# Performance work log

Hardware: AMD Instinct MI355X
Metric: run time of the kernel (lower is better)

The kernel has to match this reference:

```python
import jax, jax.numpy as jnp
import numpy as np

K = 40  # k_point

def lrelu(v):
    return jax.nn.leaky_relu(v, 0.2)

def graph_feature(x, k):
    # x: [B, C, N] -> edge features [B, 2C, N, k] = concat(x_j - x_i, x_i)
    xx = jnp.sum(x * x, axis=1)                          # [B,N]
    inner = jnp.einsum('bcn,bcm->bnm', x, x)             # [B,N,N]
    dist = 2.0 * inner - xx[:, :, None] - xx[:, None, :] # negative squared distance
    idx = jax.lax.top_k(dist, k)[1]                      # [B,N,k] nearest neighbors
    xt = jnp.transpose(x, (0, 2, 1))                     # [B,N,C]
    nbr = jax.vmap(lambda f, i: f[i])(xt, idx)           # [B,N,k,C] gather
    ctr = xt[:, :, None, :]
    feat = jnp.concatenate([nbr - ctr, jnp.broadcast_to(ctr, nbr.shape)], axis=-1)
    return jnp.transpose(feat, (0, 3, 1, 2))             # [B,2C,N,k]

def conv2(f, w):  # 1x1 conv2d, no bias
    return jnp.einsum('bcnk,oc->bonk', f, w)

def conv1(f, w):  # 1x1 conv1d, no bias
    return jnp.einsum('bcn,oc->bon', f, w)

def edge_block(x, ws, k):
    f = graph_feature(x, k)
    for w in ws:
        f = lrelu(conv2(f, w))
    return jnp.max(f, axis=-1)                           # max over k neighbors

def setup_inputs() -> dict:
    key = jax.random.key(0)
    ks = jax.random.split(key, 20)
    B, N, NCLS, NSEG, D = 8, 2048, 16, 50, 1024
    def w(kk, o, c, s=0.05):
        return jax.random.normal(kk, (o, c), jnp.float32) * s
    return {
        'x': jax.random.normal(ks[0], (B, 3, N), jnp.float32),
        'l': jax.random.uniform(ks[1], (B, NCLS), dtype=jnp.float32),
        't_c1': w(ks[2], 64, 6), 't_c2': w(ks[3], 128, 64), 't_c3': w(ks[4], 1024, 128),
        't_f1': w(ks[5], 512, 1024), 't_f2': w(ks[6], 256, 512),
        't_f3_w': w(ks[7], 9, 256, 0.01),
        't_f3_b': jnp.eye(3, dtype=jnp.float32).reshape(9),  # identity-transform init
        'b1a': w(ks[8], 64, 6), 'b1b': w(ks[9], 64, 64),
        'b2a': w(ks[10], 64, 128), 'b2b': w(ks[11], 64, 64),
        'b3a': w(ks[12], 64, 128),
        'm1': w(ks[13], D, 192), 'm2': w(ks[14], 64, NCLS),
        'h1': w(ks[15], 256, D + 256), 'h2': w(ks[16], 256, 256),
        'h3': w(ks[17], 128, 256), 'h4': w(ks[18], NSEG, 128),
    }

def reference(x, l, t_c1, t_c2, t_c3, t_f1, t_f2, t_f3_w, t_f3_b,
              b1a, b1b, b2a, b2b, b3a, m1, m2, h1, h2, h3, h4):
    B, _, N = x.shape
    # transform net on graph features of raw points
    x0 = graph_feature(x, K)                              # [B,6,N,K]
    t = lrelu(conv2(x0, t_c1))
    t = lrelu(conv2(t, t_c2))
    t = jnp.max(t, axis=-1)                               # [B,128,N]
    t = lrelu(conv1(t, t_c3))
    t = jnp.max(t, axis=-1)                               # [B,1024]
    t = lrelu(t @ t_f1.T)
    t = lrelu(t @ t_f2.T)
    T = (t @ t_f3_w.T + t_f3_b).reshape(B, 3, 3)
    x = jnp.einsum('bji,bjn->bin', T, x)                  # T^T @ x
    # edge-conv blocks
    x1 = edge_block(x, [b1a, b1b], K)                     # [B,64,N]
    x2 = edge_block(x1, [b2a, b2b], K)                    # [B,64,N]
    x3 = edge_block(x2, [b3a], K)                         # [B,64,N]
    cat = jnp.concatenate([x1, x2, x3], axis=1)           # [B,192,N]
    g = jnp.max(lrelu(conv1(cat, m1)), axis=-1, keepdims=True)  # [B,1024,1]
    lv = lrelu(jnp.einsum('bc,oc->bo', l, m2))[:, :, None]      # [B,64,1]
    glob = jnp.broadcast_to(jnp.concatenate([g, lv], axis=1), (B, g.shape[1] + 64, N))
    h = jnp.concatenate([glob, x1, x2, x3], axis=1)       # [B,1280,N]
    h = lrelu(conv1(h, h1))
    h = lrelu(conv1(h, h2))
    h = lrelu(conv1(h, h3))
    return conv1(h, h4)                                   # [B,50,N]
```

## Files before the change

kernel.cpp:

```cpp
#include <hip/hip_runtime.h>
#include <cstdint>

#define NPTS 2048
#define BATCH 8
#define KNN 40

__device__ __forceinline__ float lrelu(float v){ return fmaxf(v, 0.2f*v); }
__device__ __forceinline__ bool better(float v1,int i1,float v2,int i2){
  return (v1>v2) || (v1==v2 && i1<i2);
}
__device__ __forceinline__ float4 ld4(const float* p){ return *(const float4*)p; }

#define INSERT8(v,id,d,m) \
  if (better(d, m, v[7], id[7])){ \
    v[7]=d; id[7]=m; \
    { if (better(v[7],id[7],v[6],id[6])){ float tv=v[6];int ti=id[6]; v[6]=v[7];id[6]=id[7]; v[7]=tv;id[7]=ti; } } \
    { if (better(v[6],id[6],v[5],id[5])){ float tv=v[5];int ti=id[5]; v[5]=v[6];id[5]=id[6]; v[6]=tv;id[6]=ti; } } \
    { if (better(v[5],id[5],v[4],id[4])){ float tv=v[4];int ti=id[4]; v[4]=v[5];id[4]=id[5]; v[5]=tv;id[5]=ti; } } \
    { if (better(v[4],id[4],v[3],id[3])){ float tv=v[3];int ti=id[3]; v[3]=v[4];id[3]=id[4]; v[4]=tv;id[4]=ti; } } \
    { if (better(v[3],id[3],v[2],id[2])){ float tv=v[2];int ti=id[2]; v[2]=v[3];id[2]=id[3]; v[3]=tv;id[3]=ti; } } \
    { if (better(v[2],id[2],v[1],id[1])){ float tv=v[1];int ti=id[1]; v[1]=v[2];id[1]=id[2]; v[2]=tv;id[2]=ti; } } \
    { if (better(v[1],id[1],v[0],id[0])){ float tv=v[0];int ti=id[0]; v[0]=v[1];id[0]=id[1]; v[1]=tv;id[1]=ti; } } \
  }

__global__ void transpose_kernel(const float* __restrict__ src, float* __restrict__ dst,
                                 int R, int C, int ld, int off){
  int i = blockIdx.x*256 + threadIdx.x;
  if (i < R*C){ int r = i / C, c = i % C; dst[c*R + r] = src[r*ld + off + c]; }
}

template<int TAG>
__global__ void norms_rows_kernel(const float* __restrict__ x, float* __restrict__ xx, int N){
  int b = blockIdx.y; int n = blockIdx.x*256 + threadIdx.x;
  const float* xb = x + (size_t)b*3*N;
  float v0 = xb[n], v1 = xb[N+n], v2 = xb[2*N+n];
  xx[(size_t)b*N + n] = v0*v0 + v1*v1 + v2*v2;
}

template<int TAG>
__global__ void norms_cl_kernel(const float* __restrict__ f, int off, float* __restrict__ xx, int N){
  int b = blockIdx.y; int n = blockIdx.x*256 + threadIdx.x;
  const float4* p = (const float4*)(f + ((size_t)b*N + n)*192 + off);
  float s = 0.f;
#pragma unroll
  for (int q=0;q<16;q++){ float4 v = p[q]; s += v.x*v.x + v.y*v.y + v.z*v.z + v.w*v.w; }
  xx[(size_t)b*N + n] = s;
}

__device__ __forceinline__ void sort8(float (&v)[8], int (&id)[8]){
#define CE(a,bq) { if (better(v[bq],id[bq],v[a],id[a])){ float tv=v[a]; int ti=id[a]; v[a]=v[bq]; id[a]=id[bq]; v[bq]=tv; id[bq]=ti; } }
  CE(0,1) CE(2,3) CE(4,5) CE(6,7)
  CE(0,2) CE(1,3) CE(4,6) CE(5,7)
  CE(1,2) CE(5,6)
  CE(0,4) CE(1,5) CE(2,6) CE(3,7)
  CE(2,4) CE(3,5)
  CE(1,2) CE(3,4) CE(5,6)
#undef CE
}

template<int TAG>
__global__ __launch_bounds__(256) void knn3_kernel(
    const float* __restrict__ xrows, const float* __restrict__ xx,
    int* __restrict__ idxT, int N){
  const int b = blockIdx.y, tid = threadIdx.x;
  const int w = tid>>6, lane = tid&63;
  const int nq = blockIdx.x*4 + w;
  const float* xb = xrows + (size_t)b*3*N;
  const float* xxb = xx + (size_t)b*N;
  float c0 = xb[nq], c1 = xb[N+nq], c2 = xb[2*N+nq];
  float xxn = xxb[nq];
  float v[8]; int id[8];
#pragma unroll
  for (int j=0;j<8;j++){ v[j]=-__builtin_inff(); id[j]=0x7FFFFFFF; }
  for (int j=0;j<32;j++){
    int m = j*64 + lane;
    float s = c0*xb[m] + c1*xb[N+m] + c2*xb[2*N+m];
    float d = 2.f*s - xxn - xxb[m];
    INSERT8(v, id, d, m)
  }
  float lastv = 0.f; int lasti = 0;
  int win = 0;
  for (int r=0;r<KNN;r++){
    float bv = v[0]; int bi = id[0];
#pragma unroll
    for (int off=32; off; off>>=1){
      float ov = __shfl_xor(bv, off);
      int   oi = __shfl_xor(bi, off);
      if (better(ov, oi, bv, bi)){ bv = ov; bi = oi; }
    }
    if (lane == r) win = bi;
    if (id[0] == bi){
      lastv = v[0]; lasti = id[0];
#pragma unroll
      for (int j=0;j<7;j++){ v[j]=v[j+1]; id[j]=id[j+1]; }
      v[7] = -__builtin_inff(); id[7] = 0x7FFFFFFF;
      if (id[0] == 0x7FFFFFFF){
        float nv = -__builtin_inff(); int ni = 0x7FFFFFFF;
        for (int j=0;j<32;j++){
          int m = j*64 + lane;
          float s = c0*xb[m] + c1*xb[N+m] + c2*xb[2*N+m];
          float dd = 2.f*s - xxn - xxb[m];
          if (better(lastv, lasti, dd, m) && better(dd, m, nv, ni)){ nv=dd; ni=m; }
        }
        v[0] = nv; id[0] = ni;
      }
    }
  }
  if (lane < KNN) idxT[((size_t)b*KNN + lane)*N + nq] = win;
}

template<int TAG>
__global__ __launch_bounds__(256) void knn64_kernel(
    const float* __restrict__ featT, int featOff,
    const float* __restrict__ xx, int* __restrict__ idxT, int N){
  const int b = blockIdx.y, tid = threadIdx.x;
  const int w = tid>>6, lane = tid&63;
  __shared__ float cand[32*64];
  __shared__ float dist[4*2048];
  const float* fb = featT + featOff;
  const float* xxb = xx + (size_t)b*N;
  const int nq = blockIdx.x*4 + w;
  const int h = lane>>5;
  float4 ctr8[8];
  {
    const float4* cp = (const float4*)(fb + ((size_t)b*N + nq)*192);
#pragma unroll
    for (int q=0;q<8;q++) ctr8[q] = cp[h*8 + q];
  }
  float xxn = xxb[nq];
  float* dw = &dist[w*2048];
  float4 g[2];
#pragma unroll
  for (int r=0;r<2;r++){
    int k2 = tid + 256*r;
    int c = k2>>4, f = k2&15;
    g[r] = ld4(&fb[((size_t)b*N + c)*192 + 4*f]);
  }
  const int cc = lane&31, swz = cc&15, qb = h*8;
  for (int t=0;t<64;t++){
    __syncthreads();
#pragma unroll
    for (int r=0;r<2;r++){
      int k2 = tid + 256*r;
      int c = k2>>4, f = k2&15;
      *(float4*)&cand[(c<<6) + ((f ^ (c&15))<<2)] = g[r];
    }
    __syncthreads();
    if (t+1 < 64){
      int m0n = (t+1)*32;
#pragma unroll
      for (int r=0;r<2;r++){
        int k2 = tid + 256*r;
        int c = k2>>4, f = k2&15;
        g[r] = ld4(&fb[((size_t)b*N + m0n + c)*192 + 4*f]);
      }
    }
    float s0=0.f,s1=0.f,s2=0.f,s3=0.f;
#pragma unroll
    for (int j=0;j<8;j++){
      float4 mv = *(const float4*)&cand[(cc<<6) + (((qb + j) ^ swz)<<2)];
      s0 = fmaf(ctr8[j].x, mv.x, s0);
      s1 = fmaf(ctr8[j].y, mv.y, s1);
      s2 = fmaf(ctr8[j].z, mv.z, s2);
      s3 = fmaf(ctr8[j].w, mv.w, s3);
    }
    float p = (s0+s1)+(s2+s3);
    float tot = p + __shfl_xor(p, 32);
    if (h == (t&1)){
      int m = t*32 + cc;
      dw[(t>>1)*64 + lane] = 2.f*tot - xxn - xxb[m];
    }
  }
  float v[8]; int id[8];
#pragma unroll
  for (int j=0;j<8;j++){ v[j]=dw[j*64+lane]; id[j]=j*64+lane; }
  sort8(v, id);
#pragma unroll
  for (int gq=1; gq<4; gq++){
    float a[8]; int ai[8];
#pragma unroll
    for (int j=0;j<8;j++){ a[j]=dw[(gq*8+j)*64+lane]; ai[j]=(gq*8+j)*64+lane; }
    sort8(a, ai);
    float m_[8]; int mi_[8];
#pragma unroll
    for (int k=0;k<8;k++){
      if (better(a[7-k], ai[7-k], v[k], id[k])){ m_[k]=a[7-k]; mi_[k]=ai[7-k]; }
      else                                     { m_[k]=v[k];   mi_[k]=id[k]; }
    }
#define CEB(x,y) { if (better(m_[y],mi_[y],m_[x],mi_[x])){ float tv=m_[x];int ti=mi_[x]; m_[x]=m_[y];mi_[x]=mi_[y]; m_[y]=tv;mi_[y]=ti; } }
    CEB(0,4) CEB(1,5) CEB(2,6) CEB(3,7)
    CEB(0,2) CEB(1,3) CEB(4,6) CEB(5,7)
    CEB(0,1) CEB(2,3) CEB(4,5) CEB(6,7)
#undef CEB
#pragma unroll
    for (int k=0;k<8;k++){ v[k]=m_[k]; id[k]=mi_[k]; }
  }
  float lastv = 0.f; int lasti = 0;
  int win = 0;
  for (int r=0;r<KNN;r++){
    float bv = v[0]; int bi = id[0];
#pragma unroll
    for (int off=32; off; off>>=1){
      float ov = __shfl_xor(bv, off);
      int   oi = __shfl_xor(bi, off);
      if (better(ov, oi, bv, bi)){ bv = ov; bi = oi; }
    }
    if (lane == r) win = bi;
    if (id[0] == bi){
      lastv = v[0]; lasti = id[0];
#pragma unroll
      for (int j=0;j<7;j++){ v[j]=v[j+1]; id[j]=id[j+1]; }
      v[7] = -__builtin_inff(); id[7] = 0x7FFFFFFF;
      if (id[0] == 0x7FFFFFFF){
        float nv = -__builtin_inff(); int ni = 0x7FFFFFFF;
        for (int j=0;j<32;j++){
          float vv = dw[j*64 + lane]; int m = j*64 + lane;
          if (better(lastv, lasti, vv, m) && better(vv, m, nv, ni)){ nv=vv; ni=m; }
        }
        v[0] = nv; id[0] = ni;
      }
    }
  }
  if (lane < KNN) idxT[((size_t)b*KNN + lane)*N + nq] = win;
}


__global__ __launch_bounds__(256) void edgeA_kernel(
    const float* __restrict__ x, const int* __restrict__ idxT,
    const float* __restrict__ w1, const float* __restrict__ w2,
    float* __restrict__ tT, int N){
  __shared__ float w1aT[3*64];
  __shared__ float wd3T[3*64];
  __shared__ float w2T[64*128];
  __shared__ float aT3[4][3*16];
  __shared__ float s1T[4][64*16];
  const int tid = threadIdx.x, w = tid>>6, lane = tid&63;
  const int oq = lane&7, rg = lane>>3;
  const int o0 = oq*8, r0 = rg*2;
  const int b = blockIdx.y, n0 = blockIdx.x*16;
  for (int i=tid; i<192; i+=256){
    int o = i&63, c = i/64;
    float a = w1[o*6+c];
    w1aT[c*64+o] = a; wd3T[c*64+o] = w1[o*6+3+c] - a;
  }
  for (int i=tid; i<128*64; i+=256){
    int o = i>>6, c = i&63;
    w2T[c*128+o] = w2[o*64+c];
  }
  if (tid < 48){ int c = tid>>4, r = tid&15; aT3[0][c*16+r] = x[((size_t)b*3+c)*N + n0 + r]; }
  __syncthreads();
  float base[16];
#pragma unroll
  for (int i=0;i<16;i++) base[i]=0.f;
#pragma unroll
  for (int c=0;c<3;c++){
    float4 wA = ld4(&wd3T[c*64+o0]), wB = ld4(&wd3T[c*64+o0+4]);
    float2 av = *(const float2*)&aT3[0][c*16+r0];
    float wv[8] = {wA.x,wA.y,wA.z,wA.w,wB.x,wB.y,wB.z,wB.w};
    float rv[2] = {av.x,av.y};
#pragma unroll
    for (int oo=0;oo<8;oo++)
#pragma unroll
      for (int rr=0;rr<2;rr++) base[oo*2+rr] = fmaf(wv[oo], rv[rr], base[oo*2+rr]);
  }
  __syncthreads();
  float mx[32];
#pragma unroll
  for (int i=0;i<32;i++) mx[i] = -__builtin_inff();
  for (int it=0; it<10; it++){
    int k = it*4 + w;
    int m = idxT[((size_t)b*KNN + k)*N + n0 + (lane&15)];
    if (lane < 48){ int c = lane>>4; aT3[w][c*16 + (lane&15)] = x[((size_t)b*3+c)*N + m]; }
    float acc[16];
#pragma unroll
    for (int i=0;i<16;i++) acc[i] = base[i];
#pragma unroll
    for (int c=0;c<3;c++){
      float4 wA = ld4(&w1aT[c*64+o0]), wB = ld4(&w1aT[c*64+o0+4]);
      float2 av = *(const float2*)&aT3[w][c*16+r0];
      float wv[8] = {wA.x,wA.y,wA.z,wA.w,wB.x,wB.y,wB.z,wB.w};
      float rv[2] = {av.x,av.y};
#pragma unroll
      for (int oo=0;oo<8;oo++)
#pragma unroll
        for (int rr=0;rr<2;rr++) acc[oo*2+rr] = fmaf(wv[oo], rv[rr], acc[oo*2+rr]);
    }
#pragma unroll
    for (int oo=0;oo<8;oo++){
      float2 sv; sv.x = lrelu(acc[oo*2]); sv.y = lrelu(acc[oo*2+1]);
      *(float2*)&s1T[w][(o0+oo)*16 + r0] = sv;
    }
    float acc2[32];
#pragma unroll
    for (int i=0;i<32;i++) acc2[i]=0.f;
    for (int c=0;c<64;c++){
      float2 av = *(const float2*)&s1T[w][c*16 + r0];
#pragma unroll
      for (int p=0;p<4;p++){
        float4 wv = ld4(&w2T[c*128 + p*32 + oq*4]);
        acc2[p*8+0] = fmaf(wv.x, av.x, acc2[p*8+0]);
        acc2[p*8+1] = fmaf(wv.x, av.y, acc2[p*8+1]);
        acc2[p*8+2] = fmaf(wv.y, av.x, acc2[p*8+2]);
        acc2[p*8+3] = fmaf(wv.y, av.y, acc2[p*8+3]);
        acc2[p*8+4] = fmaf(wv.z, av.x, acc2[p*8+4]);
        acc2[p*8+5] = fmaf(wv.z, av.y, acc2[p*8+5]);
        acc2[p*8+6] = fmaf(wv.w, av.x, acc2[p*8+6]);
        acc2[p*8+7] = fmaf(wv.w, av.y, acc2[p*8+7]);
      }
    }
#pragma unroll
    for (int i=0;i<32;i++) mx[i] = fmaxf(mx[i], lrelu(acc2[i]));
  }
  __syncthreads();
#pragma unroll
  for (int rr=0;rr<2;rr++){
#pragma unroll
    for (int p=0;p<4;p++){
      float4 a = make_float4(mx[p*8+0+rr], mx[p*8+2+rr], mx[p*8+4+rr], mx[p*8+6+rr]);
      *(float4*)&w2T[w*2048 + (r0+rr)*128 + p*32 + oq*4] = a;
    }
  }
  __syncthreads();
  for (int i=tid; i<2048; i+=256){
    float vv = fmaxf(fmaxf(w2T[i], w2T[2048+i]), fmaxf(w2T[4096+i], w2T[6144+i]));
    int r = i>>7, o = i&127;
    tT[((size_t)b*N + n0 + r)*128 + o] = vv;
  }
}

__global__ __launch_bounds__(128) void edgeB_kernel(
    const float* __restrict__ xp, const int* __restrict__ idxT,
    const float* __restrict__ w1, const float* __restrict__ w2,
    float* __restrict__ catT, int N){
  __shared__ float w1aT[3*64];
  __shared__ float wd3T[3*64];
  __shared__ float w2T[64*64];
  __shared__ float aT3[2][3*32];
  __shared__ float s1T[2][64*32];
  const int tid = threadIdx.x, w = tid>>6, lane = tid&63;
  const int oq = lane&7, rg = lane>>3;
  const int o0 = oq*8, r0 = rg*4;
  const int b = blockIdx.y, n0 = blockIdx.x*32;
  for (int i=tid; i<192; i+=128){
    int o = i&63, c = i>>6;
    float a = w1[o*6+c], bb = w1[o*6+3+c];
    w1aT[c*64+o] = a; wd3T[c*64+o] = bb - a;
  }
  for (int i=tid; i<64*64; i+=128){
    int o = i>>6, c = i&63;
    w2T[c*64+o] = w2[o*64+c];
  }
  if (tid < 32){
#pragma unroll
    for (int c=0;c<3;c++) aT3[0][c*32+tid] = xp[((size_t)b*3+c)*N + n0 + tid];
  }
  __syncthreads();
  float base[32];
#pragma unroll
  for (int i=0;i<32;i++) base[i]=0.f;
#pragma unroll
  for (int c=0;c<3;c++){
    float4 w0 = ld4(&wd3T[c*64+o0]), w1v = ld4(&wd3T[c*64+o0+4]);
    float4 av = ld4(&aT3[0][c*32+r0]);
    float wv[8] = {w0.x,w0.y,w0.z,w0.w,w1v.x,w1v.y,w1v.z,w1v.w};
    float rv[4] = {av.x,av.y,av.z,av.w};
#pragma unroll
    for (int oo=0;oo<8;oo++)
#pragma unroll
      for (int rr=0;rr<4;rr++) base[oo*4+rr] = fmaf(wv[oo], rv[rr], base[oo*4+rr]);
  }
  __syncthreads();
  float mx[32];
#pragma unroll
  for (int i=0;i<32;i++) mx[i] = -__builtin_inff();
  for (int it=0; it<20; it++){
    int k = it*2 + w;
    {
      int row = lane&31;
      int m = idxT[((size_t)b*KNN + k)*N + n0 + row];
      if (lane < 32){
#pragma unroll
        for (int c=0;c<3;c++) aT3[w][c*32+row] = xp[((size_t)b*3+c)*N + m];
      }
    }
    float acc[32];
#pragma unroll
    for (int i=0;i<32;i++) acc[i] = base[i];
#pragma unroll
    for (int c=0;c<3;c++){
      float4 w0 = ld4(&w1aT[c*64+o0]), w1v = ld4(&w1aT[c*64+o0+4]);
      float4 av = ld4(&aT3[w][c*32+r0]);
      float wv[8] = {w0.x,w0.y,w0.z,w0.w,w1v.x,w1v.y,w1v.z,w1v.w};
      float rv[4] = {av.x,av.y,av.z,av.w};
#pragma unroll
      for (int oo=0;oo<8;oo++)
#pragma unroll
        for (int rr=0;rr<4;rr++) acc[oo*4+rr] = fmaf(wv[oo], rv[rr], acc[oo*4+rr]);
    }
#pragma unroll
    for (int oo=0;oo<8;oo++){
      float4 sv = make_float4(lrelu(acc[oo*4+0]), lrelu(acc[oo*4+1]), lrelu(acc[oo*4+2]), lrelu(acc[oo*4+3]));
      *(float4*)&s1T[w][(o0+oo)*32 + r0] = sv;
    }
    float acc2[32];
#pragma unroll
    for (int i=0;i<32;i++) acc2[i]=0.f;
    for (int c=0;c<64;c++){
      float4 w0 = ld4(&w2T[c*64+o0]), w1v = ld4(&w2T[c*64+o0+4]);
      float4 av = ld4(&s1T[w][c*32+r0]);
      float wv[8] = {w0.x,w0.y,w0.z,w0.w,w1v.x,w1v.y,w1v.z,w1v.w};
      float rv[4] = {av.x,av.y,av.z,av.w};
#pragma unroll
      for (int oo=0;oo<8;oo++)
#pragma unroll
        for (int rr=0;rr<4;rr++) acc2[oo*4+rr] = fmaf(wv[oo], rv[rr], acc2[oo*4+rr]);
    }
#pragma unroll
    for (int i=0;i<32;i++) mx[i] = fmaxf(mx[i], lrelu(acc2[i]));
  }
  __syncthreads();
#pragma unroll
  for (int rr=0;rr<4;rr++){
    float4 a = make_float4(mx[0*4+rr], mx[1*4+rr], mx[2*4+rr], mx[3*4+rr]);
    float4 bq = make_float4(mx[4*4+rr], mx[5*4+rr], mx[6*4+rr], mx[7*4+rr]);
    *(float4*)&s1T[w][(r0+rr)*64 + o0] = a;
    *(float4*)&s1T[w][(r0+rr)*64 + o0 + 4] = bq;
  }
  __syncthreads();
  for (int i=tid; i<2048; i+=128){
    float v = fmaxf(s1T[0][i], s1T[1][i]);
    int r = i>>6, o = i&63;
    catT[((size_t)b*N + n0 + r)*192 + o] = v;
  }
}

__global__ __launch_bounds__(128) void edgeC_kernel(
    const float* __restrict__ inT, int inOff, const int* __restrict__ idxT,
    const float* __restrict__ w1, const float* __restrict__ w2,
    float* __restrict__ catT, int outOff, int N){
  __shared__ float w1T[64*64];
  __shared__ float w2T[64*64];
  __shared__ float aT[2][64*32];
  __shared__ float s1T[2][64*32];
  const int tid = threadIdx.x, w = tid>>6, lane = tid&63;
  const int oq = lane&7, rg = lane>>3;
  const int o0 = oq*8, r0 = rg*4;
  const int b = blockIdx.y, n0 = blockIdx.x*32;
  for (int i=tid; i<64*64; i+=128){
    int o = i>>6, c = i&63;
    float a = w1[o*128+c], bb = w1[o*128+64+c];
    w1T[c*64+o] = a; w2T[c*64+o] = bb - a;
  }
  for (int i=tid; i<512; i+=128){
    int p = i>>4, cq = i&15;
    float4 v = ld4(&inT[((size_t)b*N + n0 + p)*192 + inOff + cq*4]);
    aT[0][(cq*4+0)*32+p] = v.x; aT[0][(cq*4+1)*32+p] = v.y;
    aT[0][(cq*4+2)*32+p] = v.z; aT[0][(cq*4+3)*32+p] = v.w;
  }
  __syncthreads();
  float base[32];
#pragma unroll
  for (int i=0;i<32;i++) base[i]=0.f;
  for (int c=0;c<64;c++){
    float4 w0 = ld4(&w2T[c*64+o0]), w1v = ld4(&w2T[c*64+o0+4]);
    float4 av = ld4(&aT[0][c*32+r0]);
    float wv[8] = {w0.x,w0.y,w0.z,w0.w,w1v.x,w1v.y,w1v.z,w1v.w};
    float rv[4] = {av.x,av.y,av.z,av.w};
#pragma unroll
    for (int oo=0;oo<8;oo++)
#pragma unroll
      for (int rr=0;rr<4;rr++) base[oo*4+rr] = fmaf(wv[oo], rv[rr], base[oo*4+rr]);
  }
  __syncthreads();
  for (int i=tid; i<64*64; i+=128){
    int o = i>>6, c = i&63;
    w2T[c*64+o] = w2[o*64+c];
  }
  __syncthreads();
  float mx[32];
#pragma unroll
  for (int i=0;i<32;i++) mx[i] = -__builtin_inff();
  const int row = lane&31, ch = lane>>5;
  for (int it=0; it<20; it++){
    int k = it*2 + w;
    {
      int m = idxT[((size_t)b*KNN + k)*N + n0 + row];
      const float* src = &inT[((size_t)b*N + m)*192 + inOff + ch*32];
      float4 g[8];
#pragma unroll
      for (int j=0;j<8;j++) g[j] = ld4(src + j*4);
#pragma unroll
      for (int j=0;j<8;j++){
        aT[w][(ch*32+j*4+0)*32 + row] = g[j].x;
        aT[w][(ch*32+j*4+1)*32 + row] = g[j].y;
        aT[w][(ch*32+j*4+2)*32 + row] = g[j].z;
        aT[w][(ch*32+j*4+3)*32 + row] = g[j].w;
      }
    }
    float acc[32];
#pragma unroll
    for (int i=0;i<32;i++) acc[i] = base[i];
    for (int c=0;c<64;c++){
      float4 w0 = ld4(&w1T[c*64+o0]), w1v = ld4(&w1T[c*64+o0+4]);
      float4 av = ld4(&aT[w][c*32+r0]);
      float wv[8] = {w0.x,w0.y,w0.z,w0.w,w1v.x,w1v.y,w1v.z,w1v.w};
      float rv[4] = {av.x,av.y,av.z,av.w};
#pragma unroll
      for (int oo=0;oo<8;oo++)
#pragma unroll
        for (int rr=0;rr<4;rr++) acc[oo*4+rr] = fmaf(wv[oo], rv[rr], acc[oo*4+rr]);
    }
#pragma unroll
    for (int oo=0;oo<8;oo++){
      float4 sv = make_float4(lrelu(acc[oo*4+0]), lrelu(acc[oo*4+1]), lrelu(acc[oo*4+2]), lrelu(acc[oo*4+3]));
      *(float4*)&s1T[w][(o0+oo)*32 + r0] = sv;
    }
    float acc2[32];
#pragma unroll
    for (int i=0;i<32;i++) acc2[i]=0.f;
    for (int c=0;c<64;c++){
      float4 w0 = ld4(&w2T[c*64+o0]), w1v = ld4(&w2T[c*64+o0+4]);
      float4 av = ld4(&s1T[w][c*32+r0]);
      float wv[8] = {w0.x,w0.y,w0.z,w0.w,w1v.x,w1v.y,w1v.z,w1v.w};
      float rv[4] = {av.x,av.y,av.z,av.w};
#pragma unroll
      for (int oo=0;oo<8;oo++)
#pragma unroll
        for (int rr=0;rr<4;rr++) acc2[oo*4+rr] = fmaf(wv[oo], rv[rr], acc2[oo*4+rr]);
    }
#pragma unroll
    for (int i=0;i<32;i++) mx[i] = fmaxf(mx[i], lrelu(acc2[i]));
  }
  __syncthreads();
#pragma unroll
  for (int rr=0;rr<4;rr++){
    float4 a = make_float4(mx[0*4+rr], mx[1*4+rr], mx[2*4+rr], mx[3*4+rr]);
    float4 bq = make_float4(mx[4*4+rr], mx[5*4+rr], mx[6*4+rr], mx[7*4+rr]);
    *(float4*)&s1T[w][(r0+rr)*64 + o0] = a;
    *(float4*)&s1T[w][(r0+rr)*64 + o0 + 4] = bq;
  }
  __syncthreads();
  for (int i=tid; i<2048; i+=128){
    float v = fmaxf(s1T[0][i], s1T[1][i]);
    int r = i>>6, o = i&63;
    catT[((size_t)b*N + n0 + r)*192 + outOff + o] = v;
  }
}

__global__ __launch_bounds__(128) void edgeD_kernel(
    const float* __restrict__ inT, int inOff, const int* __restrict__ idxT,
    const float* __restrict__ w1, float* __restrict__ catT, int outOff, int N){
  __shared__ float w1T[64*64];
  __shared__ float wdT[64*64];
  __shared__ float aT[2][64*32];
  const int tid = threadIdx.x, w = tid>>6, lane = tid&63;
  const int oq = lane&7, rg = lane>>3;
  const int o0 = oq*8, r0 = rg*4;
  const int b = blockIdx.y, n0 = blockIdx.x*32;
  for (int i=tid; i<64*64; i+=128){
    int o = i>>6, c = i&63;
    float a = w1[o*128+c], bb = w1[o*128+64+c];
    w1T[c*64+o] = a; wdT[c*64+o] = bb - a;
  }
  for (int i=tid; i<512; i+=128){
    int p = i>>4, cq = i&15;
    float4 v = ld4(&inT[((size_t)b*N + n0 + p)*192 + inOff + cq*4]);
    aT[0][(cq*4+0)*32+p] = v.x; aT[0][(cq*4+1)*32+p] = v.y;
    aT[0][(cq*4+2)*32+p] = v.z; aT[0][(cq*4+3)*32+p] = v.w;
  }
  __syncthreads();
  float base[32];
#pragma unroll
  for (int i=0;i<32;i++) base[i]=0.f;
  for (int c=0;c<64;c++){
    float4 w0 = ld4(&wdT[c*64+o0]), w1v = ld4(&wdT[c*64+o0+4]);
    float4 av = ld4(&aT[0][c*32+r0]);
    float wv[8] = {w0.x,w0.y,w0.z,w0.w,w1v.x,w1v.y,w1v.z,w1v.w};
    float rv[4] = {av.x,av.y,av.z,av.w};
#pragma unroll
    for (int oo=0;oo<8;oo++)
#pragma unroll
      for (int rr=0;rr<4;rr++) base[oo*4+rr] = fmaf(wv[oo], rv[rr], base[oo*4+rr]);
  }
  __syncthreads();
  float mx[32];
#pragma unroll
  for (int i=0;i<32;i++) mx[i] = -__builtin_inff();
  const int row = lane&31, ch = lane>>5;
  for (int it=0; it<20; it++){
    int k = it*2 + w;
    {
      int m = idxT[((size_t)b*KNN + k)*N + n0 + row];
      const float* src = &inT[((size_t)b*N + m)*192 + inOff + ch*32];
      float4 g[8];
#pragma unroll
      for (int j=0;j<8;j++) g[j] = ld4(src + j*4);
#pragma unroll
      for (int j=0;j<8;j++){
        aT[w][(ch*32+j*4+0)*32 + row] = g[j].x;
        aT[w][(ch*32+j*4+1)*32 + row] = g[j].y;
        aT[w][(ch*32+j*4+2)*32 + row] = g[j].z;
        aT[w][(ch*32+j*4+3)*32 + row] = g[j].w;
      }
    }
    float acc[32];
#pragma unroll
    for (int i=0;i<32;i++) acc[i] = base[i];
    for (int c=0;c<64;c++){
      float4 w0 = ld4(&w1T[c*64+o0]), w1v = ld4(&w1T[c*64+o0+4]);
      float4 av = ld4(&aT[w][c*32+r0]);
      float wv[8] = {w0.x,w0.y,w0.z,w0.w,w1v.x,w1v.y,w1v.z,w1v.w};
      float rv[4] = {av.x,av.y,av.z,av.w};
#pragma unroll
      for (int oo=0;oo<8;oo++)
#pragma unroll
        for (int rr=0;rr<4;rr++) acc[oo*4+rr] = fmaf(wv[oo], rv[rr], acc[oo*4+rr]);
    }
#pragma unroll
    for (int i=0;i<32;i++) mx[i] = fmaxf(mx[i], lrelu(acc[i]));
  }
  __syncthreads();
#pragma unroll
  for (int rr=0;rr<4;rr++){
    float4 a = make_float4(mx[0*4+rr], mx[1*4+rr], mx[2*4+rr], mx[3*4+rr]);
    float4 bq = make_float4(mx[4*4+rr], mx[5*4+rr], mx[6*4+rr], mx[7*4+rr]);
    *(float4*)&wdT[w*2048 + (r0+rr)*64 + o0] = a;
    *(float4*)&wdT[w*2048 + (r0+rr)*64 + o0 + 4] = bq;
  }
  __syncthreads();
  for (int i=tid; i<2048; i+=128){
    float v = fmaxf(wdT[i], wdT[2048+i]);
    int r = i>>6, o = i&63;
    catT[((size_t)b*N + n0 + r)*192 + outOff + o] = v;
  }
}

template<int CIN, int TAG>
__global__ __launch_bounds__(128) void convmax_kernel(
    const float* __restrict__ inT, const float* __restrict__ wT,
    float* __restrict__ partial, int N){
  __shared__ float wsh[CIN*64];
  __shared__ float ish[2][32*CIN];
  const int tid = threadIdx.x, w = tid>>6, lane = tid&63;
  const int oq = lane&7, rg = lane>>3;
  const int o0 = oq*8, r0 = rg*4;
  const int b = blockIdx.z, oc = blockIdx.x, nt = blockIdx.y;
  for (int i=tid; i<CIN*64; i+=128){
    int c = i>>6, o = i&63;
    wsh[i] = wT[(size_t)c*1024 + oc*64 + o];
  }
  __syncthreads();
  float mx[32];
#pragma unroll
  for (int i=0;i<32;i++) mx[i] = -__builtin_inff();
  const int nbase = nt*(N/8);
  float* mish = ish[w];
  for (int it=0; it<4; it++){
    const int st = it*2 + w;
    const float* src = inT + ((size_t)b*N + nbase + st*32)*CIN;
    for (int i=lane; i<32*(CIN/4); i+=64){
      int p = i/(CIN/4), cq = i%(CIN/4);
      float4 v = ld4(src + p*CIN + 4*cq);
      int base = (((p>>2) ^ (cq&7))<<2) + (p&3);
      mish[(4*cq+0)*32 + base] = v.x;
      mish[(4*cq+1)*32 + base] = v.y;
      mish[(4*cq+2)*32 + base] = v.z;
      mish[(4*cq+3)*32 + base] = v.w;
    }
    float acc[32];
#pragma unroll
    for (int i=0;i<32;i++) acc[i]=0.f;
    for (int c=0;c<CIN;c++){
      float4 w0 = ld4(&wsh[c*64+o0]), w1v = ld4(&wsh[c*64+o0+4]);
      float4 av = ld4(&mish[c*32 + ((rg ^ ((c>>2)&7))<<2)]);
      float wv[8] = {w0.x,w0.y,w0.z,w0.w,w1v.x,w1v.y,w1v.z,w1v.w};
      float rv[4] = {av.x,av.y,av.z,av.w};
#pragma unroll
      for (int oo=0;oo<8;oo++)
#pragma unroll
        for (int rr=0;rr<4;rr++) acc[oo*4+rr] = fmaf(wv[oo], rv[rr], acc[oo*4+rr]);
    }
#pragma unroll
    for (int i=0;i<32;i++) mx[i] = fmaxf(mx[i], lrelu(acc[i]));
  }
  float m8[8];
#pragma unroll
  for (int oo=0;oo<8;oo++)
    m8[oo] = fmaxf(fmaxf(mx[oo*4+0], mx[oo*4+1]), fmaxf(mx[oo*4+2], mx[oo*4+3]));
  __syncthreads();
  float* mb = ish[0];
  *(float4*)&mb[(w*8+rg)*64 + o0]     = make_float4(m8[0],m8[1],m8[2],m8[3]);
  *(float4*)&mb[(w*8+rg)*64 + o0 + 4] = make_float4(m8[4],m8[5],m8[6],m8[7]);
  __syncthreads();
  if (tid < 64){
    float v = -__builtin_inff();
#pragma unroll
    for (int g=0; g<16; g++) v = fmaxf(v, mb[g*64+tid]);
    partial[((size_t)b*8 + nt)*1024 + oc*64 + tid] = v;
  }
}

template<int TAG>
__global__ void reduce_max_kernel(const float* __restrict__ partial, float* __restrict__ out){
  int b = blockIdx.y; int o = blockIdx.x*256 + threadIdx.x;
  float v = -__builtin_inff();
  for (int s=0;s<8;s++) v = fmaxf(v, partial[((size_t)b*8 + s)*1024 + o]);
  out[(size_t)b*1024 + o] = v;
}

__global__ void fc_kernel(const float* __restrict__ in, const float* __restrict__ W,
                          const float* __restrict__ bias, float* __restrict__ out,
                          int CI, int O, int act){
  int b = blockIdx.x;
  __shared__ float insh[1024];
  for (int i=threadIdx.x;i<CI;i+=blockDim.x) insh[i]=in[(size_t)b*CI+i];
  __syncthreads();
  for (int o=threadIdx.x;o<O;o+=blockDim.x){
    float s = bias ? bias[o] : 0.f;
    for (int c=0;c<CI;c++) s = fmaf(W[(size_t)o*CI+c], insh[c], s);
    if (act) s = lrelu(s);
    out[(size_t)b*O+o]=s;
  }
}

__global__ void transform_kernel(const float* __restrict__ x, const float* __restrict__ T9,
                                 float* __restrict__ xp, int N){
  int b = blockIdx.y; int n = blockIdx.x*256 + threadIdx.x;
  const float* t = T9 + (size_t)b*9;
  float x0=x[((size_t)b*3+0)*N+n], x1=x[((size_t)b*3+1)*N+n], x2=x[((size_t)b*3+2)*N+n];
#pragma unroll
  for (int i=0;i<3;i++)
    xp[((size_t)b*3+i)*N+n] = t[i]*x0 + t[3+i]*x1 + t[6+i]*x2;
}

__global__ void bias1_kernel(const float* __restrict__ g, const float* __restrict__ lv,
                             const float* __restrict__ h1w, float* __restrict__ bias1){
  int b = blockIdx.x;
  __shared__ float insh[1088];
  for (int i=threadIdx.x;i<1088;i+=256) insh[i] = (i<1024)? g[(size_t)b*1024+i] : lv[(size_t)b*64 + (i-1024)];
  __syncthreads();
  int o = threadIdx.x;
  float s=0.f;
  for (int c=0;c<1088;c++) s = fmaf(h1w[(size_t)o*1280+c], insh[c], s);
  bias1[(size_t)b*256+o]=s;
}

template<int CI, int O, bool ACT>
__global__ __launch_bounds__(128) void conv1_kernel(
    const float* __restrict__ inT, const float* __restrict__ wT,
    const float* __restrict__ bias, float* __restrict__ outT, int N){
  constexpr int CCH = (CI % 128 == 0) ? 128 : 96;
  constexpr int NCH = CI / CCH;
  __shared__ float wsh[CCH*64];
  __shared__ float ish[32*CCH];
  const int tid = threadIdx.x, w = tid>>6, lane = tid&63;
  const int oq = lane&7, rg = lane>>3;
  const int o0 = oq*8, r0 = w*16 + rg*2;
  const int b = blockIdx.y, n0 = blockIdx.x*32, oc = blockIdx.z;
  const float* src = inT + ((size_t)b*N + n0)*CI;
  float acc[16];
#pragma unroll
  for (int i=0;i<16;i++) acc[i]=0.f;
  for (int ch=0; ch<NCH; ch++){
    const int cc0 = ch*CCH;
    if (ch) __syncthreads();
    for (int i=tid; i<CCH*64; i+=128){
      int c = i>>6, od = i&63;
      wsh[i] = wT[(size_t)(cc0+c)*O + oc*64 + od];
    }
    for (int i=tid; i<32*(CCH/4); i+=128){
      int p = i/(CCH/4), cq = i%(CCH/4);
      float4 v = ld4(src + p*CI + cc0 + 4*cq);
      int base = (((p>>2) ^ (cq&7))<<2) + (p&3);
      ish[(4*cq+0)*32 + base] = v.x;
      ish[(4*cq+1)*32 + base] = v.y;
      ish[(4*cq+2)*32 + base] = v.z;
      ish[(4*cq+3)*32 + base] = v.w;
    }
    __syncthreads();
    for (int c=0;c<CCH;c++){
      float4 w0 = ld4(&wsh[c*64+o0]), w1v = ld4(&wsh[c*64+o0+4]);
      float2 av = *(const float2*)&ish[c*32 + ((((r0>>2) ^ ((c>>2)&7))<<2) + (r0&3))];
      float wv[8] = {w0.x,w0.y,w0.z,w0.w,w1v.x,w1v.y,w1v.z,w1v.w};
      float rv[2] = {av.x,av.y};
#pragma unroll
      for (int oo=0;oo<8;oo++)
#pragma unroll
        for (int rr=0;rr<2;rr++) acc[oo*2+rr] = fmaf(wv[oo], rv[rr], acc[oo*2+rr]);
    }
  }
  float bv[8];
  if (bias){
    float4 b0 = ld4(&bias[(size_t)b*O + oc*64 + o0]);
    float4 b1 = ld4(&bias[(size_t)b*O + oc*64 + o0 + 4]);
    bv[0]=b0.x; bv[1]=b0.y; bv[2]=b0.z; bv[3]=b0.w;
    bv[4]=b1.x; bv[5]=b1.y; bv[6]=b1.z; bv[7]=b1.w;
  } else {
#pragma unroll
    for (int i=0;i<8;i++) bv[i]=0.f;
  }
#pragma unroll
  for (int rr=0;rr<2;rr++){
    float oa[8];
#pragma unroll
    for (int oo=0;oo<8;oo++){
      float s = acc[oo*2+rr] + bv[oo];
      oa[oo] = ACT ? lrelu(s) : s;
    }
    float* dst = &outT[((size_t)b*N + n0 + r0 + rr)*O + oc*64 + o0];
    *(float4*)dst     = make_float4(oa[0],oa[1],oa[2],oa[3]);
    *(float4*)(dst+4) = make_float4(oa[4],oa[5],oa[6],oa[7]);
  }
}

__global__ __launch_bounds__(256) void conv_out_kernel(
    const float* __restrict__ inT, const float* __restrict__ wT,
    float* __restrict__ out, int N){
  const int b = blockIdx.y, n0 = blockIdx.x*32;
  __shared__ float insh[32*129];
  const float* src = inT + ((size_t)b*N + n0)*128;
  for (int i=threadIdx.x;i<32*128;i+=256){ int nn=i>>7, c=i&127; insh[nn*129+c]=src[i]; }
  __syncthreads();
  const int nl = threadIdx.x & 31, og = threadIdx.x >> 5;
  float acc[7];
#pragma unroll
  for (int t=0;t<7;t++) acc[t]=0.f;
  for (int c=0;c<128;c++){
    float iv = insh[nl*129+c];
#pragma unroll
    for (int t=0;t<7;t++){
      int o = og + 8*t;
      float wv = (o<50)? wT[c*50+o] : 0.f;
      acc[t] = fmaf(wv, iv, acc[t]);
    }
  }
#pragma unroll
  for (int t=0;t<7;t++){
    int o = og + 8*t;
    if (o < 50) out[((size_t)b*50+o)*N + n0 + nl] = acc[t];
  }
}

extern "C" void kernel_launch(void* const* d_in, const int* in_sizes, int n_in,
                              void* d_out, int out_size, void* d_ws, size_t ws_size,
                              hipStream_t stream){
  const float* x    = (const float*)d_in[0];
  const float* l    = (const float*)d_in[1];
  const float* t_c1 = (const float*)d_in[2];
  const float* t_c2 = (const float*)d_in[3];
  const float* t_c3 = (const float*)d_in[4];
  const float* t_f1 = (const float*)d_in[5];
  const float* t_f2 = (const float*)d_in[6];
  const float* t_f3w= (const float*)d_in[7];
  const float* t_f3b= (const float*)d_in[8];
  const float* b1a  = (const float*)d_in[9];
  const float* b1b  = (const float*)d_in[10];
  const float* b2a  = (const float*)d_in[11];
  const float* b2b  = (const float*)d_in[12];
  const float* b3a  = (const float*)d_in[13];
  const float* m1   = (const float*)d_in[14];
  const float* m2   = (const float*)d_in[15];
  const float* h1   = (const float*)d_in[16];
  const float* h2   = (const float*)d_in[17];
  const float* h3   = (const float*)d_in[18];
  const float* h4   = (const float*)d_in[19];
  float* out = (float*)d_out;
  float* ws = (float*)d_ws;
  const int N = NPTS, B = BATCH;

  size_t off = 0;
  auto alloc = [&](size_t nf){ float* p = ws + off; off += nf; return p; };
  float* WT_TC3 = alloc((size_t)128*1024);
  float* WT_M1  = alloc((size_t)192*1024);
  float* WT_H1B = alloc((size_t)192*256);
  float* WT_H2  = alloc((size_t)256*256);
  float* WT_H3  = alloc((size_t)256*128);
  float* WT_H4  = alloc((size_t)128*64);
  int*   IDXT   = (int*)alloc((size_t)B*N*KNN);
  float* XX     = alloc((size_t)B*N);
  float* TT     = alloc((size_t)B*N*128);
  float* PARTIAL= alloc((size_t)B*8*1024);
  float* TG     = alloc((size_t)B*1024);
  float* T512   = alloc((size_t)B*512);
  float* T256   = alloc((size_t)B*256);
  float* T9     = alloc((size_t)B*16);
  float* XP     = alloc((size_t)B*3*N);
  float* CATT   = alloc((size_t)B*N*192);
  float* G      = alloc((size_t)B*1024);
  float* LV     = alloc((size_t)B*64);
  float* BIAS1  = alloc((size_t)B*256);
  float* H1T    = alloc((size_t)B*N*256);
  float* H2T    = alloc((size_t)B*N*256);
  float* H3T    = alloc((size_t)B*N*128);
  (void)ws_size; (void)in_sizes; (void)n_in; (void)out_size;

  dim3 blk(256);
  dim3 eblk(128);
  transpose_kernel<<<dim3((1024*128+255)/256), blk, 0, stream>>>(t_c3, WT_TC3, 1024,128,128,0);
  transpose_kernel<<<dim3((1024*192+255)/256), blk, 0, stream>>>(m1,  WT_M1, 1024,192,192,0);
  transpose_kernel<<<dim3((256*192+255)/256),  blk, 0, stream>>>(h1, WT_H1B, 256,192,1280,1088);
  transpose_kernel<<<dim3((256*256+255)/256),  blk, 0, stream>>>(h2, WT_H2, 256,256,256,0);
  transpose_kernel<<<dim3((128*256+255)/256),  blk, 0, stream>>>(h3, WT_H3, 128,256,256,0);
  transpose_kernel<<<dim3((50*128+255)/256),   blk, 0, stream>>>(h4, WT_H4, 50,128,128,0);

  norms_rows_kernel<0><<<dim3(N/256,B), blk, 0, stream>>>(x, XX, N);
  knn3_kernel<0><<<dim3(N/4,B), blk, 0, stream>>>(x, XX, IDXT, N);
  edgeA_kernel<<<dim3(N/16,B), blk, 0, stream>>>(x, IDXT, t_c1, t_c2, TT, N);
  convmax_kernel<128,0><<<dim3(16,8,B), eblk, 0, stream>>>(TT, WT_TC3, PARTIAL, N);
  reduce_max_kernel<0><<<dim3(4,B), blk, 0, stream>>>(PARTIAL, TG);
  fc_kernel<<<dim3(B), dim3(512), 0, stream>>>(TG, t_f1, nullptr, T512, 1024, 512, 1);
  fc_kernel<<<dim3(B), dim3(512), 0, stream>>>(T512, t_f2, nullptr, T256, 512, 256, 1);
  fc_kernel<<<dim3(B), dim3(512), 0, stream>>>(T256, t_f3w, t_f3b, T9, 256, 9, 0);
  transform_kernel<<<dim3(N/256,B), blk, 0, stream>>>(x, T9, XP, N);

  norms_rows_kernel<1><<<dim3(N/256,B), blk, 0, stream>>>(XP, XX, N);
  knn3_kernel<1><<<dim3(N/4,B), blk, 0, stream>>>(XP, XX, IDXT, N);
  edgeB_kernel<<<dim3(N/32,B), eblk, 0, stream>>>(XP, IDXT, b1a, b1b, CATT, N);

  norms_cl_kernel<0><<<dim3(N/256,B), blk, 0, stream>>>(CATT, 0, XX, N);
  knn64_kernel<0><<<dim3(N/4,B), blk, 0, stream>>>(CATT, 0, XX, IDXT, N);
  edgeC_kernel<<<dim3(N/32,B), eblk, 0, stream>>>(CATT, 0, IDXT, b2a, b2b, CATT, 64, N);

  norms_cl_kernel<1><<<dim3(N/256,B), blk, 0, stream>>>(CATT, 64, XX, N);
  knn64_kernel<1><<<dim3(N/4,B), blk, 0, stream>>>(CATT, 64, XX, IDXT, N);
  edgeD_kernel<<<dim3(N/32,B), eblk, 0, stream>>>(CATT, 64, IDXT, b3a, CATT, 128, N);

  convmax_kernel<192,1><<<dim3(16,8,B), eblk, 0, stream>>>(CATT, WT_M1, PARTIAL, N);
  reduce_max_kernel<1><<<dim3(4,B), blk, 0, stream>>>(PARTIAL, G);
  fc_kernel<<<dim3(B), dim3(512), 0, stream>>>(l, m2, nullptr, LV, 16, 64, 1);
  bias1_kernel<<<dim3(B), blk, 0, stream>>>(G, LV, h1, BIAS1);
  conv1_kernel<192,256,true><<<dim3(N/32,B,4), eblk, 0, stream>>>(CATT, WT_H1B, BIAS1, H1T, N);
  conv1_kernel<256,256,true><<<dim3(N/32,B,4), eblk, 0, stream>>>(H1T, WT_H2, nullptr, H2T, N);
  conv1_kernel<256,128,true><<<dim3(N/32,B,2), eblk, 0, stream>>>(H2T, WT_H3, nullptr, H3T, N);
  conv_out_kernel<<<dim3(N/32,B), blk, 0, stream>>>(H3T, WT_H4, out, N);
}
```

Measured before the change: 2.326 ms.

## Merge small launches and prefetch neighbor gathers in edge-conv loops

Merges the six weight transposes into one kernel, fuses the three T-Net FC layers into one kernel, and folds the label FC into bias1, which cuts about eight small kernel launches. The edge-conv kernels now load the next neighbor's gathered features into registers while the current iteration computes, so gather latency overlaps the FMA work. The prefetch raises register pressure, which may lower occupancy. The fused FC kernel runs only one block per batch element, so little parallelism is available to it.

```diff
diff --git a/kernel.cpp b/kernel.cpp
--- a/kernel.cpp
+++ b/kernel.cpp
@@ -23,9 +23,23 @@
     { if (better(v[1],id[1],v[0],id[0])){ float tv=v[0];int ti=id[0]; v[0]=v[1];id[0]=id[1]; v[1]=tv;id[1]=ti; } } \
   }
 
-__global__ void transpose_kernel(const float* __restrict__ src, float* __restrict__ dst,
-                                 int R, int C, int ld, int off){
+__global__ void transpose6_kernel(
+    const float* __restrict__ s0, float* __restrict__ d0,
+    const float* __restrict__ s1, float* __restrict__ d1,
+    const float* __restrict__ s2, float* __restrict__ d2,
+    const float* __restrict__ s3, float* __restrict__ d3,
+    const float* __restrict__ s4, float* __restrict__ d4,
+    const float* __restrict__ s5, float* __restrict__ d5){
   int i = blockIdx.x*256 + threadIdx.x;
+  const float* src; float* dst; int R,C,ld,off;
+  switch (blockIdx.y){
+    case 0:  src=s0; dst=d0; R=1024; C=128; ld=128;  off=0;    break;
+    case 1:  src=s1; dst=d1; R=1024; C=192; ld=192;  off=0;    break;
+    case 2:  src=s2; dst=d2; R=256;  C=192; ld=1280; off=1088; break;
+    case 3:  src=s3; dst=d3; R=256;  C=256; ld=256;  off=0;    break;
+    case 4:  src=s4; dst=d4; R=128;  C=256; ld=256;  off=0;    break;
+    default: src=s5; dst=d5; R=50;   C=128; ld=128;  off=0;    break;
+  }
   if (i < R*C){ int r = i / C, c = i % C; dst[c*R + r] = src[r*ld + off + c]; }
 }
 
@@ -373,14 +387,28 @@
   float mx[32];
 #pragma unroll
   for (int i=0;i<32;i++) mx[i] = -__builtin_inff();
+  const int row = lane&31;
+  float g0=0.f, g1=0.f, g2=0.f;
+  {
+    int m = idxT[((size_t)b*KNN + w)*N + n0 + row];
+    if (lane < 32){
+      g0 = xp[((size_t)b*3+0)*N + m];
+      g1 = xp[((size_t)b*3+1)*N + m];
+      g2 = xp[((size_t)b*3+2)*N + m];
+    }
+  }
   for (int it=0; it<20; it++){
-    int k = it*2 + w;
-    {
-      int row = lane&31;
-      int m = idxT[((size_t)b*KNN + k)*N + n0 + row];
+    if (lane < 32){
+      aT3[w][0*32+row] = g0;
+      aT3[w][1*32+row] = g1;
+      aT3[w][2*32+row] = g2;
+    }
+    if (it+1 < 20){
+      int m = idxT[((size_t)b*KNN + (it+1)*2 + w)*N + n0 + row];
       if (lane < 32){
-#pragma unroll
-        for (int c=0;c<3;c++) aT3[w][c*32+row] = xp[((size_t)b*3+c)*N + m];
+        g0 = xp[((size_t)b*3+0)*N + m];
+        g1 = xp[((size_t)b*3+1)*N + m];
+        g2 = xp[((size_t)b*3+2)*N + m];
       }
     }
     float acc[32];
@@ -481,21 +509,26 @@
 #pragma unroll
   for (int i=0;i<32;i++) mx[i] = -__builtin_inff();
   const int row = lane&31, ch = lane>>5;
+  float4 g[8];
+  {
+    int m = idxT[((size_t)b*KNN + w)*N + n0 + row];
+    const float* src = &inT[((size_t)b*N + m)*192 + inOff + ch*32];
+#pragma unroll
+    for (int j=0;j<8;j++) g[j] = ld4(src + j*4);
+  }
   for (int it=0; it<20; it++){
-    int k = it*2 + w;
-    {
-      int m = idxT[((size_t)b*KNN + k)*N + n0 + row];
+#pragma unroll
+    for (int j=0;j<8;j++){
+      aT[w][(ch*32+j*4+0)*32 + row] = g[j].x;
+      aT[w][(ch*32+j*4+1)*32 + row] = g[j].y;
+      aT[w][(ch*32+j*4+2)*32 + row] = g[j].z;
+      aT[w][(ch*32+j*4+3)*32 + row] = g[j].w;
+    }
+    if (it+1 < 20){
+      int m = idxT[((size_t)b*KNN + (it+1)*2 + w)*N + n0 + row];
       const float* src = &inT[((size_t)b*N + m)*192 + inOff + ch*32];
-      float4 g[8];
 #pragma unroll
       for (int j=0;j<8;j++) g[j] = ld4(src + j*4);
-#pragma unroll
-      for (int j=0;j<8;j++){
-        aT[w][(ch*32+j*4+0)*32 + row] = g[j].x;
-        aT[w][(ch*32+j*4+1)*32 + row] = g[j].y;
-        aT[w][(ch*32+j*4+2)*32 + row] = g[j].z;
-        aT[w][(ch*32+j*4+3)*32 + row] = g[j].w;
-      }
     }
     float acc[32];
 #pragma unroll
@@ -587,21 +620,26 @@
 #pragma unroll
   for (int i=0;i<32;i++) mx[i] = -__builtin_inff();
   const int row = lane&31, ch = lane>>5;
+  float4 g[8];
+  {
+    int m = idxT[((size_t)b*KNN + w)*N + n0 + row];
+    const float* src = &inT[((size_t)b*N + m)*192 + inOff + ch*32];
+#pragma unroll
+    for (int j=0;j<8;j++) g[j] = ld4(src + j*4);
+  }
   for (int it=0; it<20; it++){
-    int k = it*2 + w;
-    {
-      int m = idxT[((size_t)b*KNN + k)*N + n0 + row];
+#pragma unroll
+    for (int j=0;j<8;j++){
+      aT[w][(ch*32+j*4+0)*32 + row] = g[j].x;
+      aT[w][(ch*32+j*4+1)*32 + row] = g[j].y;
+      aT[w][(ch*32+j*4+2)*32 + row] = g[j].z;
+      aT[w][(ch*32+j*4+3)*32 + row] = g[j].w;
+    }
+    if (it+1 < 20){
+      int m = idxT[((size_t)b*KNN + (it+1)*2 + w)*N + n0 + row];
       const float* src = &inT[((size_t)b*N + m)*192 + inOff + ch*32];
-      float4 g[8];
 #pragma unroll
       for (int j=0;j<8;j++) g[j] = ld4(src + j*4);
-#pragma unroll
-      for (int j=0;j<8;j++){
-        aT[w][(ch*32+j*4+0)*32 + row] = g[j].x;
-        aT[w][(ch*32+j*4+1)*32 + row] = g[j].y;
-        aT[w][(ch*32+j*4+2)*32 + row] = g[j].z;
-        aT[w][(ch*32+j*4+3)*32 + row] = g[j].w;
-      }
     }
     float acc[32];
 #pragma unroll
@@ -643,7 +681,7 @@
   __shared__ float ish[2][32*CIN];
   const int tid = threadIdx.x, w = tid>>6, lane = tid&63;
   const int oq = lane&7, rg = lane>>3;
-  const int o0 = oq*8, r0 = rg*4;
+  const int o0 = oq*8;
   const int b = blockIdx.z, oc = blockIdx.x, nt = blockIdx.y;
   for (int i=tid; i<CIN*64; i+=128){
     int c = i>>6, o = i&63;
@@ -708,18 +746,32 @@
   out[(size_t)b*1024 + o] = v;
 }
 
-__global__ void fc_kernel(const float* __restrict__ in, const float* __restrict__ W,
-                          const float* __restrict__ bias, float* __restrict__ out,
-                          int CI, int O, int act){
-  int b = blockIdx.x;
-  __shared__ float insh[1024];
-  for (int i=threadIdx.x;i<CI;i+=blockDim.x) insh[i]=in[(size_t)b*CI+i];
-  __syncthreads();
-  for (int o=threadIdx.x;o<O;o+=blockDim.x){
-    float s = bias ? bias[o] : 0.f;
-    for (int c=0;c<CI;c++) s = fmaf(W[(size_t)o*CI+c], insh[c], s);
-    if (act) s = lrelu(s);
-    out[(size_t)b*O+o]=s;
+__global__ __launch_bounds__(512) void tnet_fc_kernel(
+    const float* __restrict__ tg, const float* __restrict__ t_f1,
+    const float* __restrict__ t_f2, const float* __restrict__ t_f3w,
+    const float* __restrict__ t_f3b, float* __restrict__ T9){
+  const int b = blockIdx.x, tid = threadIdx.x;
+  __shared__ float in1[1024];
+  __shared__ float h512[512];
+  __shared__ float h256[256];
+  for (int i=tid;i<1024;i+=512) in1[i] = tg[(size_t)b*1024+i];
+  __syncthreads();
+  {
+    float s = 0.f;
+    for (int c=0;c<1024;c++) s = fmaf(t_f1[(size_t)tid*1024+c], in1[c], s);
+    h512[tid] = lrelu(s);
+  }
+  __syncthreads();
+  if (tid < 256){
+    float s = 0.f;
+    for (int c=0;c<512;c++) s = fmaf(t_f2[(size_t)tid*512+c], h512[c], s);
+    h256[tid] = lrelu(s);
+  }
+  __syncthreads();
+  if (tid < 9){
+    float s = t_f3b[tid];
+    for (int c=0;c<256;c++) s = fmaf(t_f3w[(size_t)tid*256+c], h256[c], s);
+    T9[(size_t)b*9+tid] = s;
   }
 }
 
@@ -733,11 +785,18 @@
     xp[((size_t)b*3+i)*N+n] = t[i]*x0 + t[3+i]*x1 + t[6+i]*x2;
 }
 
-__global__ void bias1_kernel(const float* __restrict__ g, const float* __restrict__ lv,
-                             const float* __restrict__ h1w, float* __restrict__ bias1){
+__global__ void bias1_kernel(const float* __restrict__ g, const float* __restrict__ l,
+                             const float* __restrict__ m2, const float* __restrict__ h1w,
+                             float* __restrict__ bias1){
   int b = blockIdx.x;
   __shared__ float insh[1088];
-  for (int i=threadIdx.x;i<1088;i+=256) insh[i] = (i<1024)? g[(size_t)b*1024+i] : lv[(size_t)b*64 + (i-1024)];
+  for (int i=threadIdx.x;i<1024;i+=256) insh[i] = g[(size_t)b*1024+i];
+  if (threadIdx.x < 64){
+    int o = threadIdx.x;
+    float s = 0.f;
+    for (int c=0;c<16;c++) s = fmaf(m2[(size_t)o*16+c], l[(size_t)b*16+c], s);
+    insh[1024+o] = lrelu(s);
+  }
   __syncthreads();
   int o = threadIdx.x;
   float s=0.f;
@@ -881,13 +940,10 @@
   float* TT     = alloc((size_t)B*N*128);
   float* PARTIAL= alloc((size_t)B*8*1024);
   float* TG     = alloc((size_t)B*1024);
-  float* T512   = alloc((size_t)B*512);
-  float* T256   = alloc((size_t)B*256);
   float* T9     = alloc((size_t)B*16);
   float* XP     = alloc((size_t)B*3*N);
   float* CATT   = alloc((size_t)B*N*192);
   float* G      = alloc((size_t)B*1024);
-  float* LV     = alloc((size_t)B*64);
   float* BIAS1  = alloc((size_t)B*256);
   float* H1T    = alloc((size_t)B*N*256);
   float* H2T    = alloc((size_t)B*N*256);
@@ -896,21 +952,15 @@
 
   dim3 blk(256);
   dim3 eblk(128);
-  transpose_kernel<<<dim3((1024*128+255)/256), blk, 0, stream>>>(t_c3, WT_TC3, 1024,128,128,0);
-  transpose_kernel<<<dim3((1024*192+255)/256), blk, 0, stream>>>(m1,  WT_M1, 1024,192,192,0);
-  transpose_kernel<<<dim3((256*192+255)/256),  blk, 0, stream>>>(h1, WT_H1B, 256,192,1280,1088);
-  transpose_kernel<<<dim3((256*256+255)/256),  blk, 0, stream>>>(h2, WT_H2, 256,256,256,0);
-  transpose_kernel<<<dim3((128*256+255)/256),  blk, 0, stream>>>(h3, WT_H3, 128,256,256,0);
-  transpose_kernel<<<dim3((50*128+255)/256),   blk, 0, stream>>>(h4, WT_H4, 50,128,128,0);
+  transpose6_kernel<<<dim3(768,6), blk, 0, stream>>>(
+      t_c3, WT_TC3, m1, WT_M1, h1, WT_H1B, h2, WT_H2, h3, WT_H3, h4, WT_H4);
 
   norms_rows_kernel<0><<<dim3(N/256,B), blk, 0, stream>>>(x, XX, N);
   knn3_kernel<0><<<dim3(N/4,B), blk, 0, stream>>>(x, XX, IDXT, N);
   edgeA_kernel<<<dim3(N/16,B), blk, 0, stream>>>(x, IDXT, t_c1, t_c2, TT, N);
   convmax_kernel<128,0><<<dim3(16,8,B), eblk, 0, stream>>>(TT, WT_TC3, PARTIAL, N);
   reduce_max_kernel<0><<<dim3(4,B), blk, 0, stream>>>(PARTIAL, TG);
-  fc_kernel<<<dim3(B), dim3(512), 0, stream>>>(TG, t_f1, nullptr, T512, 1024, 512, 1);
-  fc_kernel<<<dim3(B), dim3(512), 0, stream>>>(T512, t_f2, nullptr, T256, 512, 256, 1);
-  fc_kernel<<<dim3(B), dim3(512), 0, stream>>>(T256, t_f3w, t_f3b, T9, 256, 9, 0);
+  tnet_fc_kernel<<<dim3(B), dim3(512), 0, stream>>>(TG, t_f1, t_f2, t_f3w, t_f3b, T9);
   transform_kernel<<<dim3(N/256,B), blk, 0, stream>>>(x, T9, XP, N);
 
   norms_rows_kernel<1><<<dim3(N/256,B), blk, 0, stream>>>(XP, XX, N);
@@ -927,8 +977,7 @@
 
   convmax_kernel<192,1><<<dim3(16,8,B), eblk, 0, stream>>>(CATT, WT_M1, PARTIAL, N);
   reduce_max_kernel<1><<<dim3(4,B), blk, 0, stream>>>(PARTIAL, G);
-  fc_kernel<<<dim3(B), dim3(512), 0, stream>>>(l, m2, nullptr, LV, 16, 64, 1);
-  bias1_kernel<<<dim3(B), blk, 0, stream>>>(G, LV, h1, BIAS1);
+  bias1_kernel<<<dim3(B), blk, 0, stream>>>(G, l, m2, h1, BIAS1);
   conv1_kernel<192,256,true><<<dim3(N/32,B,4), eblk, 0, stream>>>(CATT, WT_H1B, BIAS1, H1T, N);
   conv1_kernel<256,256,true><<<dim3(N/32,B,4), eblk, 0, stream>>>(H1T, WT_H2, nullptr, H2T, N);
   conv1_kernel<256,128,true><<<dim3(N/32,B,2), eblk, 0, stream>>>(H2T, WT_H3, nullptr, H3T, N);
```

Result: no change. 2.297 ms (-1.3%).
